# Performance work log

Measured on AMD Instinct MI355X. Metric: run time of the kernel, lower is better.

## Reference

```python
import jax, jax.numpy as jnp
import numpy as np

B, S, EMB, HID, IMG, ATT, K, HL = 64, 512, 768, 512, 2048, 512, 6, 20


def setup_inputs() -> dict:
    key = jax.random.key(0)
    ks = jax.random.split(key, 14)
    u = lambda k, shape: jax.random.uniform(k, shape, jnp.float32, -0.1, 0.1)
    return {
        "representations": jax.random.normal(ks[0], (B, S, EMB), jnp.float32),
        "lengths": jax.random.randint(ks[1], (B,), 0, S),
        "separate_images": jax.random.normal(ks[2], (B, K, IMG), jnp.float32),
        "visual_context": jax.random.normal(ks[3], (B, K * IMG), jnp.float32),
        "prev_hist": jax.random.normal(ks[4], (B, K, HL, EMB), jnp.float32),
        "hist_counts": jax.random.randint(ks[5], (B, K), 0, HL + 1),
        "masks": jax.random.randint(ks[6], (B, S, 1), 0, 2).astype(bool),
        "W_sep": u(ks[7], (IMG, HID)), "b_sep": jnp.zeros((HID,), jnp.float32),
        "W_e2h": u(ks[8], (EMB, HID)), "b_e2h": jnp.zeros((HID,), jnp.float32),
        "W_hist": u(ks[9], (EMB, HID)), "b_hist": jnp.zeros((HID,), jnp.float32),
        "W_ctx": u(ks[10], (K * IMG, HID)), "b_ctx": jnp.zeros((HID,), jnp.float32),
        "W_mm": u(ks[11], (2 * HID, HID)), "b_mm": jnp.zeros((HID,), jnp.float32),
        "W_a1": u(ks[12], (HID, ATT)), "b_a1": jnp.zeros((ATT,), jnp.float32),
        "W_a2": u(ks[13], (ATT, 1)), "b_a2": jnp.zeros((1,), jnp.float32),
    }


def reference(representations, lengths, separate_images, visual_context,
              prev_hist, hist_counts, masks,
              W_sep, b_sep, W_e2h, b_e2h, W_hist, b_hist, W_ctx, b_ctx,
              W_mm, b_mm, W_a1, b_a1, W_a2, b_a2):
    # dropout_prob = 0 -> dropout is identity (eval-mode equivalence)
    input_reps = jax.nn.relu(representations @ W_e2h + b_e2h)          # [B,S,H]
    ctx = jax.nn.relu(visual_context @ W_ctx + b_ctx)                  # [B,H]
    ctx_rep = jnp.broadcast_to(ctx[:, None, :], input_reps.shape)
    mm = jax.nn.relu(jnp.concatenate([input_reps, ctx_rep], -1) @ W_mm + b_mm)  # [B,S,H]
    scores = jnp.tanh(mm @ W_a1 + b_a1) @ W_a2 + b_a2                  # [B,S,1]
    scores = jnp.where(masks, -jnp.inf, scores)
    att_w = jax.nn.softmax(scores, axis=1)                             # softmax over seq
    attended = jnp.sum(mm * att_w, axis=1)                             # [B,H]

    sep = separate_images @ W_sep + b_sep                              # [B,K,H]
    hl = prev_hist.shape[2]
    valid = jnp.arange(hl)[None, None, :] < hist_counts[:, :, None]    # [B,K,HL]
    hsum = jnp.sum(prev_hist * valid[..., None].astype(prev_hist.dtype), axis=2)
    havg = hsum / jnp.maximum(hist_counts, 1)[..., None].astype(prev_hist.dtype)
    hproj = jax.nn.relu(havg @ W_hist + b_hist)                        # [B,K,H]
    sep = sep + jnp.where((hist_counts > 0)[..., None], hproj, 0.0)
    sep = jax.nn.relu(sep)
    # F.normalize(p=2, dim=2, eps=1e-12)
    sep = sep / jnp.maximum(jnp.linalg.norm(sep, axis=2, keepdims=True), 1e-12)
    dot = jnp.einsum('bkh,bh->bk', sep, attended)[..., None]           # [B,K,1]
    return dot
```

## Files before the change

kernel.cpp:

```cpp
#include <hip/hip_runtime.h>
#include <math.h>

#define B_    64
#define S_    512
#define EMB_  768
#define HID_  512
#define IMG_  2048
#define ATT_  512
#define K_    6
#define HL_   20
#define MS_   (B_ * S_)

typedef __attribute__((ext_vector_type(8))) short bf16x8;
typedef __attribute__((ext_vector_type(4))) float f32x4;

__device__ __forceinline__ unsigned short f2b(float f) {
    unsigned int u = __float_as_uint(f);
    u += 0x7fffu + ((u >> 16) & 1u);
    return (unsigned short)(u >> 16);
}
__device__ __forceinline__ unsigned int pk_bf16(float lo, float hi) {
    unsigned int r;
    asm volatile("v_cvt_pk_bf16_f32 %0, %1, %2" : "=v"(r) : "v"(lo), "v"(hi));
    return r;
}

#define GLD_LDS16(gp, lp)                                                        \
    __builtin_amdgcn_global_load_lds(                                            \
        (const __attribute__((address_space(1))) void*)(gp),                     \
        (__attribute__((address_space(3))) void*)(lp), 16, 0, 0)

__global__ __launch_bounds__(256)
void prep(const float* __restrict__ W_e2h, const float* __restrict__ W_mm,
          const float* __restrict__ W_a1,
          unsigned short* __restrict__ WtE2H, unsigned short* __restrict__ WtMM,
          unsigned short* __restrict__ WtA1,
          const unsigned char* __restrict__ masks, int* __restrict__ flag) {
    const int z = blockIdx.z;
    if (z == 3) {
        if (blockIdx.x != 0 || blockIdx.y != 0) return;
        __shared__ int found;
        if (threadIdx.x == 0) found = 0;
        __syncthreads();
        for (int i = threadIdx.x; i < 8192; i += 256)
            if ((i & 3) != 0 && masks[i] != 0) found = 1;
        __syncthreads();
        if (threadIdx.x == 0) *flag = found;
        return;
    }
    const float* W;
    unsigned short* Wt;
    int Kd;
    if (z == 0)      { W = W_e2h; Wt = WtE2H; Kd = EMB_; }
    else if (z == 1) { W = W_mm;  Wt = WtMM;  Kd = HID_; }
    else             { W = W_a1;  Wt = WtA1;  Kd = HID_; }
    if ((int)blockIdx.x * 32 >= Kd) return;

    __shared__ float tile[32][33];
    int k0 = blockIdx.x * 32, n0 = blockIdx.y * 32;
    int tx = threadIdx.x & 31, ty = threadIdx.x >> 5;
    #pragma unroll
    for (int i = 0; i < 4; ++i)
        tile[ty + i * 8][tx] = W[(size_t)(k0 + ty + i * 8) * HID_ + n0 + tx];
    __syncthreads();
    #pragma unroll
    for (int i = 0; i < 4; ++i)
        Wt[(size_t)(n0 + ty + i * 8) * Kd + k0 + tx] = f2b(tile[tx][ty + i * 8]);
}

__device__ __forceinline__ void tile_coords(int N, int& bm, int& bn) {
    const int nwg = gridDim.x;
    const int cpx = nwg >> 3;
    const int lid = ((int)blockIdx.x & 7) * cpx + ((int)blockIdx.x >> 3);
    const int ntl = N >> 7;
    bn = (lid % ntl) << 7;
    bm = (lid / ntl) << 7;
}

template<int ACT>
__global__ __launch_bounds__(256)
void gemm_bf16(const unsigned short* __restrict__ A, const unsigned short* __restrict__ Bt,
               const float* __restrict__ bias, const float* __restrict__ row_add,
               int row_div, unsigned short* __restrict__ Co, int M, int N, int Kd) {
    __shared__ unsigned short Als[2][128 * 64];
    __shared__ unsigned short Bls[2][128 * 64];
    const int tid = threadIdx.x;
    int bm, bn; tile_coords(N, bm, bn);
    const int lane = tid & 63, wid = tid >> 6;
    const int wr = wid >> 1, wc = wid & 1;
    const int fr = lane & 15, hi = lane >> 4;

    f32x4 acc[4][4] = {};
    int srow[4], scol[4];
    #pragma unroll
    for (int c = 0; c < 4; ++c) {
        int g = c * 256 + tid;
        srow[c] = g >> 3;
        scol[c] = (g & 7) ^ (srow[c] & 7);
    }

    const int nt = Kd >> 6;
    #pragma unroll
    for (int c = 0; c < 4; ++c) {
        int g = c * 256 + tid;
        GLD_LDS16(A + (size_t)(bm + srow[c]) * Kd + scol[c] * 8, &Als[0][g * 8]);
        GLD_LDS16(Bt + (size_t)(bn + srow[c]) * Kd + scol[c] * 8, &Bls[0][g * 8]);
    }
    __syncthreads();

    for (int t = 0; t < nt; ++t) {
        const int buf = t & 1;
        if (t + 1 < nt) {
            const int k0 = (t + 1) << 6;
            #pragma unroll
            for (int c = 0; c < 4; ++c) {
                int g = c * 256 + tid;
                GLD_LDS16(A + (size_t)(bm + srow[c]) * Kd + k0 + scol[c] * 8,
                          &Als[buf ^ 1][g * 8]);
                GLD_LDS16(Bt + (size_t)(bn + srow[c]) * Kd + k0 + scol[c] * 8,
                          &Bls[buf ^ 1][g * 8]);
            }
        }
        #pragma unroll
        for (int kk = 0; kk < 2; ++kk) {
            bf16x8 af[4], bv[4];
            #pragma unroll
            for (int m = 0; m < 4; ++m) {
                int row = wr * 64 + m * 16 + fr;
                int sc = (kk * 4 + hi) ^ (fr & 7);
                af[m] = *(const bf16x8*)&Als[buf][row * 64 + sc * 8];
            }
            #pragma unroll
            for (int n = 0; n < 4; ++n) {
                int row = wc * 64 + n * 16 + fr;
                int sc = (kk * 4 + hi) ^ (fr & 7);
                bv[n] = *(const bf16x8*)&Bls[buf][row * 64 + sc * 8];
            }
            #pragma unroll
            for (int m = 0; m < 4; ++m)
                #pragma unroll
                for (int n = 0; n < 4; ++n)
                    acc[m][n] = __builtin_amdgcn_mfma_f32_16x16x32_bf16(af[m], bv[n], acc[m][n], 0, 0, 0);
        }
        __syncthreads();
    }

    #pragma unroll
    for (int m = 0; m < 4; ++m) {
        #pragma unroll
        for (int n = 0; n < 4; ++n) {
            int col = bn + wc * 64 + n * 16 + fr;
            float badd = bias ? bias[col] : 0.f;
            #pragma unroll
            for (int r = 0; r < 4; ++r) {
                int row = bm + wr * 64 + m * 16 + hi * 4 + r;
                float x = acc[m][n][r] + badd;
                if (row_add) x += row_add[(size_t)(row / row_div) * N + col];
                if (ACT == 1) x = fmaxf(x, 0.f);
                if (ACT == 2) x = tanhf(x);
                Co[(size_t)row * N + col] = f2b(x);
            }
        }
    }
}

template<int ACT>
__global__ __launch_bounds__(256)
void gemm_f32in(const float* __restrict__ A, const unsigned short* __restrict__ Bt,
                const float* __restrict__ bias, unsigned short* __restrict__ Co,
                int M, int N, int Kd) {
    __shared__ unsigned short Als[2][128 * 64];
    __shared__ unsigned short Bls[2][128 * 64];
    const int tid = threadIdx.x;
    int bm, bn; tile_coords(N, bm, bn);
    const int lane = tid & 63, wid = tid >> 6;
    const int wr = wid >> 1, wc = wid & 1;
    const int fr = lane & 15, hi = lane >> 4;

    f32x4 acc[4][4] = {};
    int srow[4], lcol[4], scol[4];
    #pragma unroll
    for (int c = 0; c < 4; ++c) {
        int g = c * 256 + tid;
        srow[c] = g >> 3;
        lcol[c] = g & 7;
        scol[c] = lcol[c] ^ (srow[c] & 7);
    }

    const int nt = Kd >> 6;
    float4 ra[8];

    #pragma unroll
    for (int c = 0; c < 4; ++c) {
        int g = c * 256 + tid;
        GLD_LDS16(Bt + (size_t)(bn + srow[c]) * Kd + scol[c] * 8, &Bls[0][g * 8]);
        const float* p = A + (size_t)(bm + srow[c]) * Kd + lcol[c] * 8;
        ra[2 * c]     = *(const float4*)p;
        ra[2 * c + 1] = *(const float4*)(p + 4);
    }
    #pragma unroll
    for (int c = 0; c < 4; ++c) {
        uint4 u;
        u.x = pk_bf16(ra[2*c].x,   ra[2*c].y);
        u.y = pk_bf16(ra[2*c].z,   ra[2*c].w);
        u.z = pk_bf16(ra[2*c+1].x, ra[2*c+1].y);
        u.w = pk_bf16(ra[2*c+1].z, ra[2*c+1].w);
        *(uint4*)&Als[0][(srow[c] * 8 + scol[c]) * 8] = u;
    }
    __syncthreads();

    for (int t = 0; t < nt; ++t) {
        const int buf = t & 1;
        if (t + 1 < nt) {
            const int k0 = (t + 1) << 6;
            #pragma unroll
            for (int c = 0; c < 4; ++c) {
                int g = c * 256 + tid;
                GLD_LDS16(Bt + (size_t)(bn + srow[c]) * Kd + k0 + scol[c] * 8,
                          &Bls[buf ^ 1][g * 8]);
                const float* p = A + (size_t)(bm + srow[c]) * Kd + k0 + lcol[c] * 8;
                ra[2 * c]     = *(const float4*)p;
                ra[2 * c + 1] = *(const float4*)(p + 4);
            }
        }
        #pragma unroll
        for (int kk = 0; kk < 2; ++kk) {
            bf16x8 af[4], bv[4];
            #pragma unroll
            for (int m = 0; m < 4; ++m) {
                int row = wr * 64 + m * 16 + fr;
                int sc = (kk * 4 + hi) ^ (fr & 7);
                af[m] = *(const bf16x8*)&Als[buf][row * 64 + sc * 8];
            }
            #pragma unroll
            for (int n = 0; n < 4; ++n) {
                int row = wc * 64 + n * 16 + fr;
                int sc = (kk * 4 + hi) ^ (fr & 7);
                bv[n] = *(const bf16x8*)&Bls[buf][row * 64 + sc * 8];
            }
            #pragma unroll
            for (int m = 0; m < 4; ++m)
                #pragma unroll
                for (int n = 0; n < 4; ++n)
                    acc[m][n] = __builtin_amdgcn_mfma_f32_16x16x32_bf16(af[m], bv[n], acc[m][n], 0, 0, 0);
        }
        if (t + 1 < nt) {
            #pragma unroll
            for (int c = 0; c < 4; ++c) {
                uint4 u;
                u.x = pk_bf16(ra[2*c].x,   ra[2*c].y);
                u.y = pk_bf16(ra[2*c].z,   ra[2*c].w);
                u.z = pk_bf16(ra[2*c+1].x, ra[2*c+1].y);
                u.w = pk_bf16(ra[2*c+1].z, ra[2*c+1].w);
                *(uint4*)&Als[buf ^ 1][(srow[c] * 8 + scol[c]) * 8] = u;
            }
        }
        __syncthreads();
    }

    #pragma unroll
    for (int m = 0; m < 4; ++m) {
        #pragma unroll
        for (int n = 0; n < 4; ++n) {
            int col = bn + wc * 64 + n * 16 + fr;
            float badd = bias ? bias[col] : 0.f;
            #pragma unroll
            for (int r = 0; r < 4; ++r) {
                int row = bm + wr * 64 + m * 16 + hi * 4 + r;
                float x = acc[m][n][r] + badd;
                if (ACT == 1) x = fmaxf(x, 0.f);
                Co[(size_t)row * N + col] = f2b(x);
            }
        }
    }
}

__global__ __launch_bounds__(256)
void gemm_score(const unsigned short* __restrict__ A, const unsigned short* __restrict__ Bt,
                const float* __restrict__ b_a1, const float* __restrict__ W_a2,
                float* __restrict__ scores8, int M, int N, int Kd) {
    __shared__ unsigned short Als[2][128 * 64];
    __shared__ unsigned short Bls[2][128 * 64];
    const int tid = threadIdx.x;
    int bm, bn; tile_coords(N, bm, bn);
    const int lane = tid & 63, wid = tid >> 6;
    const int wr = wid >> 1, wc = wid & 1;
    const int fr = lane & 15, hi = lane >> 4;

    f32x4 acc[4][4] = {};
    int srow[4], scol[4];
    #pragma unroll
    for (int c = 0; c < 4; ++c) {
        int g = c * 256 + tid;
        srow[c] = g >> 3;
        scol[c] = (g & 7) ^ (srow[c] & 7);
    }

    const int nt = Kd >> 6;
    #pragma unroll
    for (int c = 0; c < 4; ++c) {
        int g = c * 256 + tid;
        GLD_LDS16(A + (size_t)(bm + srow[c]) * Kd + scol[c] * 8, &Als[0][g * 8]);
        GLD_LDS16(Bt + (size_t)(bn + srow[c]) * Kd + scol[c] * 8, &Bls[0][g * 8]);
    }
    __syncthreads();

    for (int t = 0; t < nt; ++t) {
        const int buf = t & 1;
        if (t + 1 < nt) {
            const int k0 = (t + 1) << 6;
            #pragma unroll
            for (int c = 0; c < 4; ++c) {
                int g = c * 256 + tid;
                GLD_LDS16(A + (size_t)(bm + srow[c]) * Kd + k0 + scol[c] * 8,
                          &Als[buf ^ 1][g * 8]);
                GLD_LDS16(Bt + (size_t)(bn + srow[c]) * Kd + k0 + scol[c] * 8,
                          &Bls[buf ^ 1][g * 8]);
            }
        }
        #pragma unroll
        for (int kk = 0; kk < 2; ++kk) {
            bf16x8 af[4], bv[4];
            #pragma unroll
            for (int m = 0; m < 4; ++m) {
                int row = wr * 64 + m * 16 + fr;
                int sc = (kk * 4 + hi) ^ (fr & 7);
                af[m] = *(const bf16x8*)&Als[buf][row * 64 + sc * 8];
            }
            #pragma unroll
            for (int n = 0; n < 4; ++n) {
                int row = wc * 64 + n * 16 + fr;
                int sc = (kk * 4 + hi) ^ (fr & 7);
                bv[n] = *(const bf16x8*)&Bls[buf][row * 64 + sc * 8];
            }
            #pragma unroll
            for (int m = 0; m < 4; ++m)
                #pragma unroll
                for (int n = 0; n < 4; ++n)
                    acc[m][n] = __builtin_amdgcn_mfma_f32_16x16x32_bf16(af[m], bv[n], acc[m][n], 0, 0, 0);
        }
        __syncthreads();
    }

    float ba[4], wa[4];
    #pragma unroll
    for (int n = 0; n < 4; ++n) {
        int col = bn + wc * 64 + n * 16 + fr;
        ba[n] = b_a1[col];
        wa[n] = W_a2[col];
    }
    const int slot = (bn >> 7) * 2 + wc;
    #pragma unroll
    for (int m = 0; m < 4; ++m) {
        #pragma unroll
        for (int r = 0; r < 4; ++r) {
            float p = 0.f;
            #pragma unroll
            for (int n = 0; n < 4; ++n)
                p += tanhf(acc[m][n][r] + ba[n]) * wa[n];
            p += __shfl_xor(p, 1, 64);
            p += __shfl_xor(p, 2, 64);
            p += __shfl_xor(p, 4, 64);
            p += __shfl_xor(p, 8, 64);
            if (fr == 0)
                scores8[(size_t)slot * M + bm + wr * 64 + m * 16 + hi * 4 + r] = p;
        }
    }
}

__global__ __launch_bounds__(256)
void gemm_splitk(const float* __restrict__ A, const float* __restrict__ W,
                 float* __restrict__ P, int M, int N, int Kd, int kps) {
    __shared__ float As[16][68];
    __shared__ float Ws[16][64];
    const int tid = threadIdx.x;
    const int bm = blockIdx.y * 64, bn = blockIdx.x * 64;
    const int ks = blockIdx.z;
    const int tx = tid & 15, ty = tid >> 4;
    const int arow = tid >> 2, akq = tid & 3;
    const int wk = tid >> 4, wnq = tid & 15;

    float acc[4][4] = {};
    const int kbeg = ks * kps, kend = kbeg + kps;

    for (int k0 = kbeg; k0 < kend; k0 += 16) {
        float4 av = *(const float4*)&A[(size_t)(bm + arow) * Kd + k0 + akq * 4];
        float4 wv = *(const float4*)&W[(size_t)(k0 + wk) * N + bn + wnq * 4];
        As[akq * 4 + 0][arow] = av.x;
        As[akq * 4 + 1][arow] = av.y;
        As[akq * 4 + 2][arow] = av.z;
        As[akq * 4 + 3][arow] = av.w;
        *(float4*)&Ws[wk][wnq * 4] = wv;
        __syncthreads();
        #pragma unroll
        for (int kk = 0; kk < 16; ++kk) {
            float4 a4 = *(const float4*)&As[kk][ty * 4];
            float4 b4 = *(const float4*)&Ws[kk][tx * 4];
            float a_[4] = {a4.x, a4.y, a4.z, a4.w};
            float b_[4] = {b4.x, b4.y, b4.z, b4.w};
            #pragma unroll
            for (int i = 0; i < 4; ++i)
                #pragma unroll
                for (int j = 0; j < 4; ++j)
                    acc[i][j] += a_[i] * b_[j];
        }
        __syncthreads();
    }

    float* Pbase = P + (size_t)ks * M * N;
    #pragma unroll
    for (int i = 0; i < 4; ++i) {
        int row = bm + ty * 4 + i;
        float4 v = {acc[i][0], acc[i][1], acc[i][2], acc[i][3]};
        *(float4*)&Pbase[(size_t)row * N + bn + tx * 4] = v;
    }
}

template<int ACT>
__global__ __launch_bounds__(256)
void reduce_k(const float* __restrict__ P, const float* __restrict__ bias,
              float* __restrict__ C, int MN, int N, int nsplit) {
    int idx = blockIdx.x * 256 + threadIdx.x;
    if (idx >= MN) return;
    float s = 0.f;
    for (int z = 0; z < nsplit; ++z) s += P[(size_t)z * MN + idx];
    if (bias) s += bias[idx & (N - 1)];
    if (ACT == 1) s = fmaxf(s, 0.f);
    C[idx] = s;
}

__global__ __launch_bounds__(256)
void softmax8(const float* __restrict__ scores8, const float* __restrict__ b_a2,
              const void* __restrict__ masks_raw, const int* __restrict__ flag,
              float* __restrict__ attw) {
    int b = blockIdx.x, tid = threadIdx.x;
    bool isb = (*flag) != 0;
    const unsigned char* mb = (const unsigned char*)masks_raw;
    const int* mi = (const int*)masks_raw;
    int lane = tid & 63, wv = tid >> 6;
    __shared__ float red[4], red2[4];
    float bias = b_a2[0];

    float m = -INFINITY;
    for (int s = tid; s < S_; s += 256) {
        int idx = b * S_ + s;
        float v = bias;
        #pragma unroll
        for (int z = 0; z < 8; ++z) v += scores8[(size_t)z * MS_ + idx];
        bool mk = isb ? (mb[idx] != 0) : (mi[idx] != 0);
        v = mk ? -INFINITY : v;
        attw[idx] = v;
        m = fmaxf(m, v);
    }
    #pragma unroll
    for (int off = 32; off; off >>= 1) m = fmaxf(m, __shfl_down(m, off, 64));
    if (lane == 0) red[wv] = m;
    __syncthreads();
    if (tid == 0) red[0] = fmaxf(fmaxf(red[0], red[1]), fmaxf(red[2], red[3]));
    __syncthreads();
    float Mx = red[0];

    float sum = 0.f;
    for (int s = tid; s < S_; s += 256) {
        int idx = b * S_ + s;
        float e = expf(attw[idx] - Mx);
        attw[idx] = e;
        sum += e;
    }
    #pragma unroll
    for (int off = 32; off; off >>= 1) sum += __shfl_down(sum, off, 64);
    if (lane == 0) red2[wv] = sum;
    __syncthreads();
    if (tid == 0) red2[0] = red2[0] + red2[1] + red2[2] + red2[3];
    __syncthreads();
    float inv = 1.f / red2[0];
    for (int s = tid; s < S_; s += 256) attw[b * S_ + s] *= inv;
}

__global__ __launch_bounds__(256)
void attended4(const unsigned short* __restrict__ mm, const float* __restrict__ attw,
               float* __restrict__ att4) {
    int b = blockIdx.x;
    int h = blockIdx.y * 256 + threadIdx.x;
    int z = blockIdx.z;
    __shared__ float w[128];
    int s0 = z * 128;
    if (threadIdx.x < 128) w[threadIdx.x] = attw[b * S_ + s0 + threadIdx.x];
    __syncthreads();
    float acc = 0.f;
    for (int s = 0; s < 128; ++s)
        acc += __uint_as_float((unsigned int)mm[((size_t)b * S_ + s0 + s) * HID_ + h] << 16) * w[s];
    att4[((size_t)z * B_ + b) * HID_ + h] = acc;
}

__global__ __launch_bounds__(256)
void hist_avg(const float* __restrict__ ph, const int* __restrict__ hcnt,
              float* __restrict__ havg) {
    int bk = blockIdx.x;
    int cnt = hcnt[bk];
    float denom = (float)(cnt > 1 ? cnt : 1);
    const float* base = ph + (size_t)bk * HL_ * EMB_;
    for (int e = threadIdx.x; e < EMB_; e += 256) {
        float s = 0.f;
        for (int l = 0; l < cnt; ++l) s += base[l * EMB_ + e];
        havg[bk * EMB_ + e] = s / denom;
    }
}

__global__ __launch_bounds__(256)
void combine_all(const float* __restrict__ skA, const float* __restrict__ skB,
                 const float* __restrict__ b_hist, const float* __restrict__ b_sep,
                 const int* __restrict__ hcnt, const float* __restrict__ att4,
                 float* __restrict__ out) {
    const int MNA = B_ * K_ * HID_;
    int bk = blockIdx.x, tid = threadIdx.x;
    int b = bk / K_;
    int cnt = hcnt[bk];
    float sq = 0.f, dt = 0.f;
    #pragma unroll
    for (int i = 0; i < HID_ / 256; ++i) {
        int h = tid + i * 256;
        size_t idx = (size_t)bk * HID_ + h;
        float hp = b_hist[h];
        #pragma unroll
        for (int z = 0; z < 8; ++z) hp += skA[(size_t)z * MNA + idx];
        hp = fmaxf(hp, 0.f);
        float sp = b_sep[h];
        #pragma unroll
        for (int z = 0; z < 16; ++z) sp += skB[(size_t)z * MNA + idx];
        float v = sp + (cnt > 0 ? hp : 0.f);
        v = fmaxf(v, 0.f);
        float at = 0.f;
        #pragma unroll
        for (int z = 0; z < 4; ++z) at += att4[((size_t)z * B_ + b) * HID_ + h];
        sq += v * v;
        dt += v * at;
    }
    #pragma unroll
    for (int off = 32; off; off >>= 1) {
        sq += __shfl_down(sq, off, 64);
        dt += __shfl_down(dt, off, 64);
    }
    __shared__ float rs[4], rd[4];
    int lane = tid & 63, wv = tid >> 6;
    if (lane == 0) { rs[wv] = sq; rd[wv] = dt; }
    __syncthreads();
    if (tid == 0) {
        float Sq = rs[0] + rs[1] + rs[2] + rs[3];
        float Dt = rd[0] + rd[1] + rd[2] + rd[3];
        float norm = fmaxf(sqrtf(Sq), 1e-12f);
        out[bk] = Dt / norm;
    }
}

extern "C" void kernel_launch(void* const* d_in, const int* in_sizes, int n_in,
                              void* d_out, int out_size, void* d_ws, size_t ws_size,
                              hipStream_t stream) {
    const float* reps     = (const float*)d_in[0];
    const float* sep_imgs = (const float*)d_in[2];
    const float* vctx     = (const float*)d_in[3];
    const float* phist    = (const float*)d_in[4];
    const int*   hcnt     = (const int*)d_in[5];
    const void*  masks    = d_in[6];
    const float* W_sep = (const float*)d_in[7];
    const float* b_sep = (const float*)d_in[8];
    const float* W_e2h = (const float*)d_in[9];
    const float* b_e2h = (const float*)d_in[10];
    const float* W_hist = (const float*)d_in[11];
    const float* b_hist = (const float*)d_in[12];
    const float* W_ctx = (const float*)d_in[13];
    const float* b_ctx = (const float*)d_in[14];
    const float* W_mm = (const float*)d_in[15];
    const float* b_mm = (const float*)d_in[16];
    const float* W_a1 = (const float*)d_in[17];
    const float* b_a1 = (const float*)d_in[18];
    const float* W_a2 = (const float*)d_in[19];
    const float* b_a2 = (const float*)d_in[20];
    float* out = (float*)d_out;

    const size_t MS = (size_t)MS_;
    const int MNA = B_ * K_ * HID_;

    unsigned short* actA  = (unsigned short*)d_ws;
    unsigned short* actB  = actA + MS * HID_;
    unsigned short* WtE2H = actB + MS * HID_;
    unsigned short* WtMM  = WtE2H + (size_t)EMB_ * HID_;
    unsigned short* WtA1  = WtMM + (size_t)HID_ * HID_;
    float* skC    = (float*)(WtA1 + (size_t)HID_ * HID_);
    float* skA    = skC + (size_t)64 * B_ * HID_;
    float* skB    = skA + (size_t)8 * MNA;
    float* scores8 = skB + (size_t)16 * MNA;
    float* attw   = scores8 + 8 * MS;
    float* att4   = attw + MS;
    float* ctx    = att4 + (size_t)4 * B_ * HID_;
    float* ctx2   = ctx + B_ * HID_;
    float* havg   = ctx2 + B_ * HID_;
    int*   flag   = (int*)(havg + (size_t)B_ * K_ * EMB_);

    prep<<<dim3(EMB_ / 32, HID_ / 32, 4), 256, 0, stream>>>(
        W_e2h, W_mm, W_a1, WtE2H, WtMM, WtA1, (const unsigned char*)masks, flag);

    {
        const int nsp = 64, kps = (K_ * IMG_) / nsp;
        gemm_splitk<<<dim3(8, 1, nsp), 256, 0, stream>>>(vctx, W_ctx, skC,
                                                         B_, HID_, K_ * IMG_, kps);
        reduce_k<1><<<(B_ * HID_ + 255) / 256, 256, 0, stream>>>(skC, b_ctx, ctx,
                                                                 B_ * HID_, HID_, nsp);
    }
    {
        const int nsp = 8, kps = HID_ / nsp;
        gemm_splitk<<<dim3(8, 1, nsp), 256, 0, stream>>>(ctx, W_mm + (size_t)HID_ * HID_,
                                                         skC, B_, HID_, HID_, kps);
        reduce_k<0><<<(B_ * HID_ + 255) / 256, 256, 0, stream>>>(skC, b_mm, ctx2,
                                                                 B_ * HID_, HID_, nsp);
    }

    const int big_grid = (MS_ / 128) * (HID_ / 128);
    gemm_f32in<1><<<big_grid, 256, 0, stream>>>(reps, WtE2H, b_e2h, actA,
                                                MS_, HID_, EMB_);
    gemm_bf16<1><<<big_grid, 256, 0, stream>>>(actA, WtMM, nullptr, ctx2, S_,
                                               actB, MS_, HID_, HID_);
    gemm_score<<<big_grid, 256, 0, stream>>>(actB, WtA1, b_a1, W_a2, scores8,
                                             MS_, ATT_, HID_);
    softmax8<<<B_, 256, 0, stream>>>(scores8, b_a2, masks, flag, attw);
    attended4<<<dim3(B_, HID_ / 256, 4), 256, 0, stream>>>(actB, attw, att4);
    hist_avg<<<B_ * K_, 256, 0, stream>>>(phist, hcnt, havg);
    gemm_splitk<<<dim3(8, 6, 8), 256, 0, stream>>>(havg, W_hist, skA,
                                                   B_ * K_, HID_, EMB_, EMB_ / 8);
    gemm_splitk<<<dim3(8, 6, 16), 256, 0, stream>>>(sep_imgs, W_sep, skB,
                                                    B_ * K_, HID_, IMG_, IMG_ / 16);
    combine_all<<<B_ * K_, 256, 0, stream>>>(skA, skB, b_hist, b_sep, hcnt,
                                             att4, out);
}
```

Measured before the change: 262.7 us.

## Replace LDS-staged GEMMs with direct global-to-register MFMA operand loads

The three big GEMMs drop shared-memory staging and barriers. Each lane now loads its MFMA A and B fragments straight from global memory into registers, with two register sets double-buffered and s_setprio raised around the MFMA bursts. The three kernels are unified into one template, and launch bounds now target 2 blocks per CU. This removes LDS traffic and __syncthreads stalls, but each wave loses cross-wave operand reuse, so it leans on L1/L2 for the shared tiles and reads with a less coalesced 16-byte-per-lane pattern.

```diff
diff --git a/kernel.cpp b/kernel.cpp
--- a/kernel.cpp
+++ b/kernel.cpp
@@ -24,11 +24,14 @@
     asm volatile("v_cvt_pk_bf16_f32 %0, %1, %2" : "=v"(r) : "v"(lo), "v"(hi));
     return r;
 }
-
-#define GLD_LDS16(gp, lp)                                                        \
-    __builtin_amdgcn_global_load_lds(                                            \
-        (const __attribute__((address_space(1))) void*)(gp),                     \
-        (__attribute__((address_space(3))) void*)(lp), 16, 0, 0)
+__device__ __forceinline__ bf16x8 cvt8(const float4& x, const float4& y) {
+    union { unsigned int u[4]; bf16x8 v; } r;
+    r.u[0] = pk_bf16(x.x, x.y);
+    r.u[1] = pk_bf16(x.z, x.w);
+    r.u[2] = pk_bf16(y.x, y.y);
+    r.u[3] = pk_bf16(y.z, y.w);
+    return r.v;
+}
 
 __global__ __launch_bounds__(256)
 void prep(const float* __restrict__ W_e2h, const float* __restrict__ W_mm,
@@ -77,293 +80,115 @@
     bm = (lid / ntl) << 7;
 }
 
-template<int ACT>
-__global__ __launch_bounds__(256)
-void gemm_bf16(const unsigned short* __restrict__ A, const unsigned short* __restrict__ Bt,
-               const float* __restrict__ bias, const float* __restrict__ row_add,
-               int row_div, unsigned short* __restrict__ Co, int M, int N, int Kd) {
-    __shared__ unsigned short Als[2][128 * 64];
-    __shared__ unsigned short Bls[2][128 * 64];
+template<bool AF32, int ACT, bool SCORE>
+__global__ __launch_bounds__(256, 2)
+void gemm_nolds(const void* __restrict__ Av, const unsigned short* __restrict__ Bt,
+                const float* __restrict__ bias, const float* __restrict__ row_add,
+                int row_div, unsigned short* __restrict__ Co,
+                const float* __restrict__ W_a2, float* __restrict__ scores8,
+                int M, int N, int Kd) {
     const int tid = threadIdx.x;
     int bm, bn; tile_coords(N, bm, bn);
     const int lane = tid & 63, wid = tid >> 6;
     const int wr = wid >> 1, wc = wid & 1;
     const int fr = lane & 15, hi = lane >> 4;
 
+    const float* pAf[4];
+    const unsigned short* pA[4];
+    const unsigned short* pB[4];
+    #pragma unroll
+    for (int m = 0; m < 4; ++m) {
+        size_t off = (size_t)(bm + wr * 64 + m * 16 + fr) * Kd + hi * 8;
+        pAf[m] = (const float*)Av + off;
+        pA[m]  = (const unsigned short*)Av + off;
+    }
+    #pragma unroll
+    for (int n = 0; n < 4; ++n)
+        pB[n] = Bt + (size_t)(bn + wc * 64 + n * 16 + fr) * Kd + hi * 8;
+
     f32x4 acc[4][4] = {};
-    int srow[4], scol[4];
-    #pragma unroll
-    for (int c = 0; c < 4; ++c) {
-        int g = c * 256 + tid;
-        srow[c] = g >> 3;
-        scol[c] = (g & 7) ^ (srow[c] & 7);
-    }
-
-    const int nt = Kd >> 6;
-    #pragma unroll
-    for (int c = 0; c < 4; ++c) {
-        int g = c * 256 + tid;
-        GLD_LDS16(A + (size_t)(bm + srow[c]) * Kd + scol[c] * 8, &Als[0][g * 8]);
-        GLD_LDS16(Bt + (size_t)(bn + srow[c]) * Kd + scol[c] * 8, &Bls[0][g * 8]);
-    }
-    __syncthreads();
-
-    for (int t = 0; t < nt; ++t) {
-        const int buf = t & 1;
-        if (t + 1 < nt) {
-            const int k0 = (t + 1) << 6;
-            #pragma unroll
-            for (int c = 0; c < 4; ++c) {
-                int g = c * 256 + tid;
-                GLD_LDS16(A + (size_t)(bm + srow[c]) * Kd + k0 + scol[c] * 8,
-                          &Als[buf ^ 1][g * 8]);
-                GLD_LDS16(Bt + (size_t)(bn + srow[c]) * Kd + k0 + scol[c] * 8,
-                          &Bls[buf ^ 1][g * 8]);
+    bf16x8 a0[4], a1[4], b0[4], b1[4];
+    float4 f0[4][2], f1[4][2];
+
+    auto load_set = [&](bf16x8 (&AS)[4], float4 (&FS)[4][2], bf16x8 (&BS)[4], int kc) {
+        #pragma unroll
+        for (int m = 0; m < 4; ++m) {
+            if (AF32) {
+                FS[m][0] = *(const float4*)(pAf[m] + kc);
+                FS[m][1] = *(const float4*)(pAf[m] + kc + 4);
+            } else {
+                AS[m] = *(const bf16x8*)(pA[m] + kc);
             }
         }
         #pragma unroll
-        for (int kk = 0; kk < 2; ++kk) {
-            bf16x8 af[4], bv[4];
+        for (int n = 0; n < 4; ++n) BS[n] = *(const bf16x8*)(pB[n] + kc);
+    };
+    auto compute_set = [&](bf16x8 (&AS)[4], float4 (&FS)[4][2], bf16x8 (&BS)[4]) {
+        bf16x8 av[4];
+        #pragma unroll
+        for (int m = 0; m < 4; ++m)
+            av[m] = AF32 ? cvt8(FS[m][0], FS[m][1]) : AS[m];
+        __builtin_amdgcn_s_setprio(1);
+        #pragma unroll
+        for (int m = 0; m < 4; ++m)
             #pragma unroll
-            for (int m = 0; m < 4; ++m) {
-                int row = wr * 64 + m * 16 + fr;
-                int sc = (kk * 4 + hi) ^ (fr & 7);
-                af[m] = *(const bf16x8*)&Als[buf][row * 64 + sc * 8];
+            for (int n = 0; n < 4; ++n)
+                acc[m][n] = __builtin_amdgcn_mfma_f32_16x16x32_bf16(av[m], BS[n], acc[m][n], 0, 0, 0);
+        __builtin_amdgcn_s_setprio(0);
+    };
+
+    const int half = Kd >> 6;
+    load_set(a0, f0, b0, 0);
+    load_set(a1, f1, b1, 32);
+    for (int i = 0; i < half; ++i) {
+        const int kc = i << 6;
+        compute_set(a0, f0, b0);
+        if (i + 1 < half) load_set(a0, f0, b0, kc + 64);
+        compute_set(a1, f1, b1);
+        if (i + 1 < half) load_set(a1, f1, b1, kc + 96);
+    }
+
+    if (SCORE) {
+        float ba[4], wa[4];
+        #pragma unroll
+        for (int n = 0; n < 4; ++n) {
+            int col = bn + wc * 64 + n * 16 + fr;
+            ba[n] = bias[col];
+            wa[n] = W_a2[col];
+        }
+        const int slot = (bn >> 7) * 2 + wc;
+        #pragma unroll
+        for (int m = 0; m < 4; ++m) {
+            #pragma unroll
+            for (int r = 0; r < 4; ++r) {
+                float p = 0.f;
+                #pragma unroll
+                for (int n = 0; n < 4; ++n)
+                    p += tanhf(acc[m][n][r] + ba[n]) * wa[n];
+                p += __shfl_xor(p, 1, 64);
+                p += __shfl_xor(p, 2, 64);
+                p += __shfl_xor(p, 4, 64);
+                p += __shfl_xor(p, 8, 64);
+                if (fr == 0)
+                    scores8[(size_t)slot * M + bm + wr * 64 + m * 16 + hi * 4 + r] = p;
             }
+        }
+    } else {
+        #pragma unroll
+        for (int m = 0; m < 4; ++m) {
             #pragma unroll
             for (int n = 0; n < 4; ++n) {
-                int row = wc * 64 + n * 16 + fr;
-                int sc = (kk * 4 + hi) ^ (fr & 7);
-                bv[n] = *(const bf16x8*)&Bls[buf][row * 64 + sc * 8];
+                int col = bn + wc * 64 + n * 16 + fr;
+                float badd = bias ? bias[col] : 0.f;
+                #pragma unroll
+                for (int r = 0; r < 4; ++r) {
+                    int row = bm + wr * 64 + m * 16 + hi * 4 + r;
+                    float x = acc[m][n][r] + badd;
+                    if (row_add) x += row_add[(size_t)(row / row_div) * N + col];
+                    if (ACT == 1) x = fmaxf(x, 0.f);
+                    Co[(size_t)row * N + col] = f2b(x);
+                }
             }
-            #pragma unroll
-            for (int m = 0; m < 4; ++m)
-                #pragma unroll
-                for (int n = 0; n < 4; ++n)
-                    acc[m][n] = __builtin_amdgcn_mfma_f32_16x16x32_bf16(af[m], bv[n], acc[m][n], 0, 0, 0);
-        }
-        __syncthreads();
-    }
-
-    #pragma unroll
-    for (int m = 0; m < 4; ++m) {
-        #pragma unroll
-        for (int n = 0; n < 4; ++n) {
-            int col = bn + wc * 64 + n * 16 + fr;
-            float badd = bias ? bias[col] : 0.f;
-            #pragma unroll
-            for (int r = 0; r < 4; ++r) {
-                int row = bm + wr * 64 + m * 16 + hi * 4 + r;
-                float x = acc[m][n][r] + badd;
-                if (row_add) x += row_add[(size_t)(row / row_div) * N + col];
-                if (ACT == 1) x = fmaxf(x, 0.f);
-                if (ACT == 2) x = tanhf(x);
-                Co[(size_t)row * N + col] = f2b(x);
-            }
-        }
-    }
-}
-
-template<int ACT>
-__global__ __launch_bounds__(256)
-void gemm_f32in(const float* __restrict__ A, const unsigned short* __restrict__ Bt,
-                const float* __restrict__ bias, unsigned short* __restrict__ Co,
-                int M, int N, int Kd) {
-    __shared__ unsigned short Als[2][128 * 64];
-    __shared__ unsigned short Bls[2][128 * 64];
-    const int tid = threadIdx.x;
-    int bm, bn; tile_coords(N, bm, bn);
-    const int lane = tid & 63, wid = tid >> 6;
-    const int wr = wid >> 1, wc = wid & 1;
-    const int fr = lane & 15, hi = lane >> 4;
-
-    f32x4 acc[4][4] = {};
-    int srow[4], lcol[4], scol[4];
-    #pragma unroll
-    for (int c = 0; c < 4; ++c) {
-        int g = c * 256 + tid;
-        srow[c] = g >> 3;
-        lcol[c] = g & 7;
-        scol[c] = lcol[c] ^ (srow[c] & 7);
-    }
-
-    const int nt = Kd >> 6;
-    float4 ra[8];
-
-    #pragma unroll
-    for (int c = 0; c < 4; ++c) {
-        int g = c * 256 + tid;
-        GLD_LDS16(Bt + (size_t)(bn + srow[c]) * Kd + scol[c] * 8, &Bls[0][g * 8]);
-        const float* p = A + (size_t)(bm + srow[c]) * Kd + lcol[c] * 8;
-        ra[2 * c]     = *(const float4*)p;
-        ra[2 * c + 1] = *(const float4*)(p + 4);
-    }
-    #pragma unroll
-    for (int c = 0; c < 4; ++c) {
-        uint4 u;
-        u.x = pk_bf16(ra[2*c].x,   ra[2*c].y);
-        u.y = pk_bf16(ra[2*c].z,   ra[2*c].w);
-        u.z = pk_bf16(ra[2*c+1].x, ra[2*c+1].y);
-        u.w = pk_bf16(ra[2*c+1].z, ra[2*c+1].w);
-        *(uint4*)&Als[0][(srow[c] * 8 + scol[c]) * 8] = u;
-    }
-    __syncthreads();
-
-    for (int t = 0; t < nt; ++t) {
-        const int buf = t & 1;
-        if (t + 1 < nt) {
-            const int k0 = (t + 1) << 6;
-            #pragma unroll
-            for (int c = 0; c < 4; ++c) {
-                int g = c * 256 + tid;
-                GLD_LDS16(Bt + (size_t)(bn + srow[c]) * Kd + k0 + scol[c] * 8,
-                          &Bls[buf ^ 1][g * 8]);
-                const float* p = A + (size_t)(bm + srow[c]) * Kd + k0 + lcol[c] * 8;
-                ra[2 * c]     = *(const float4*)p;
-                ra[2 * c + 1] = *(const float4*)(p + 4);
-            }
-        }
-        #pragma unroll
-        for (int kk = 0; kk < 2; ++kk) {
-            bf16x8 af[4], bv[4];
-            #pragma unroll
-            for (int m = 0; m < 4; ++m) {
-                int row = wr * 64 + m * 16 + fr;
-                int sc = (kk * 4 + hi) ^ (fr & 7);
-                af[m] = *(const bf16x8*)&Als[buf][row * 64 + sc * 8];
-            }
-            #pragma unroll
-            for (int n = 0; n < 4; ++n) {
-                int row = wc * 64 + n * 16 + fr;
-                int sc = (kk * 4 + hi) ^ (fr & 7);
-                bv[n] = *(const bf16x8*)&Bls[buf][row * 64 + sc * 8];
-            }
-            #pragma unroll
-            for (int m = 0; m < 4; ++m)
-                #pragma unroll
-                for (int n = 0; n < 4; ++n)
-                    acc[m][n] = __builtin_amdgcn_mfma_f32_16x16x32_bf16(af[m], bv[n], acc[m][n], 0, 0, 0);
-        }
-        if (t + 1 < nt) {
-            #pragma unroll
-            for (int c = 0; c < 4; ++c) {
-                uint4 u;
-                u.x = pk_bf16(ra[2*c].x,   ra[2*c].y);
-                u.y = pk_bf16(ra[2*c].z,   ra[2*c].w);
-                u.z = pk_bf16(ra[2*c+1].x, ra[2*c+1].y);
-                u.w = pk_bf16(ra[2*c+1].z, ra[2*c+1].w);
-                *(uint4*)&Als[buf ^ 1][(srow[c] * 8 + scol[c]) * 8] = u;
-            }
-        }
-        __syncthreads();
-    }
-
-    #pragma unroll
-    for (int m = 0; m < 4; ++m) {
-        #pragma unroll
-        for (int n = 0; n < 4; ++n) {
-            int col = bn + wc * 64 + n * 16 + fr;
-            float badd = bias ? bias[col] : 0.f;
-            #pragma unroll
-            for (int r = 0; r < 4; ++r) {
-                int row = bm + wr * 64 + m * 16 + hi * 4 + r;
-                float x = acc[m][n][r] + badd;
-                if (ACT == 1) x = fmaxf(x, 0.f);
-                Co[(size_t)row * N + col] = f2b(x);
-            }
-        }
-    }
-}
-
-__global__ __launch_bounds__(256)
-void gemm_score(const unsigned short* __restrict__ A, const unsigned short* __restrict__ Bt,
-                const float* __restrict__ b_a1, const float* __restrict__ W_a2,
-                float* __restrict__ scores8, int M, int N, int Kd) {
-    __shared__ unsigned short Als[2][128 * 64];
-    __shared__ unsigned short Bls[2][128 * 64];
-    const int tid = threadIdx.x;
-    int bm, bn; tile_coords(N, bm, bn);
-    const int lane = tid & 63, wid = tid >> 6;
-    const int wr = wid >> 1, wc = wid & 1;
-    const int fr = lane & 15, hi = lane >> 4;
-
-    f32x4 acc[4][4] = {};
-    int srow[4], scol[4];
-    #pragma unroll
-    for (int c = 0; c < 4; ++c) {
-        int g = c * 256 + tid;
-        srow[c] = g >> 3;
-        scol[c] = (g & 7) ^ (srow[c] & 7);
-    }
-
-    const int nt = Kd >> 6;
-    #pragma unroll
-    for (int c = 0; c < 4; ++c) {
-        int g = c * 256 + tid;
-        GLD_LDS16(A + (size_t)(bm + srow[c]) * Kd + scol[c] * 8, &Als[0][g * 8]);
-        GLD_LDS16(Bt + (size_t)(bn + srow[c]) * Kd + scol[c] * 8, &Bls[0][g * 8]);
-    }
-    __syncthreads();
-
-    for (int t = 0; t < nt; ++t) {
-        const int buf = t & 1;
-        if (t + 1 < nt) {
-            const int k0 = (t + 1) << 6;
-            #pragma unroll
-            for (int c = 0; c < 4; ++c) {
-                int g = c * 256 + tid;
-                GLD_LDS16(A + (size_t)(bm + srow[c]) * Kd + k0 + scol[c] * 8,
-                          &Als[buf ^ 1][g * 8]);
-                GLD_LDS16(Bt + (size_t)(bn + srow[c]) * Kd + k0 + scol[c] * 8,
-                          &Bls[buf ^ 1][g * 8]);
-            }
-        }
-        #pragma unroll
-        for (int kk = 0; kk < 2; ++kk) {
-            bf16x8 af[4], bv[4];
-            #pragma unroll
-            for (int m = 0; m < 4; ++m) {
-                int row = wr * 64 + m * 16 + fr;
-                int sc = (kk * 4 + hi) ^ (fr & 7);
-                af[m] = *(const bf16x8*)&Als[buf][row * 64 + sc * 8];
-            }
-            #pragma unroll
-            for (int n = 0; n < 4; ++n) {
-                int row = wc * 64 + n * 16 + fr;
-                int sc = (kk * 4 + hi) ^ (fr & 7);
-                bv[n] = *(const bf16x8*)&Bls[buf][row * 64 + sc * 8];
-            }
-            #pragma unroll
-            for (int m = 0; m < 4; ++m)
-                #pragma unroll
-                for (int n = 0; n < 4; ++n)
-                    acc[m][n] = __builtin_amdgcn_mfma_f32_16x16x32_bf16(af[m], bv[n], acc[m][n], 0, 0, 0);
-        }
-        __syncthreads();
-    }
-
-    float ba[4], wa[4];
-    #pragma unroll
-    for (int n = 0; n < 4; ++n) {
-        int col = bn + wc * 64 + n * 16 + fr;
-        ba[n] = b_a1[col];
-        wa[n] = W_a2[col];
-    }
-    const int slot = (bn >> 7) * 2 + wc;
-    #pragma unroll
-    for (int m = 0; m < 4; ++m) {
-        #pragma unroll
-        for (int r = 0; r < 4; ++r) {
-            float p = 0.f;
-            #pragma unroll
-            for (int n = 0; n < 4; ++n)
-                p += tanhf(acc[m][n][r] + ba[n]) * wa[n];
-            p += __shfl_xor(p, 1, 64);
-            p += __shfl_xor(p, 2, 64);
-            p += __shfl_xor(p, 4, 64);
-            p += __shfl_xor(p, 8, 64);
-            if (fr == 0)
-                scores8[(size_t)slot * M + bm + wr * 64 + m * 16 + hi * 4 + r] = p;
         }
     }
 }
@@ -616,12 +441,12 @@
     }
 
     const int big_grid = (MS_ / 128) * (HID_ / 128);
-    gemm_f32in<1><<<big_grid, 256, 0, stream>>>(reps, WtE2H, b_e2h, actA,
-                                                MS_, HID_, EMB_);
-    gemm_bf16<1><<<big_grid, 256, 0, stream>>>(actA, WtMM, nullptr, ctx2, S_,
-                                               actB, MS_, HID_, HID_);
-    gemm_score<<<big_grid, 256, 0, stream>>>(actB, WtA1, b_a1, W_a2, scores8,
-                                             MS_, ATT_, HID_);
+    gemm_nolds<true, 1, false><<<big_grid, 256, 0, stream>>>(
+        reps, WtE2H, b_e2h, nullptr, 1, actA, nullptr, nullptr, MS_, HID_, EMB_);
+    gemm_nolds<false, 1, false><<<big_grid, 256, 0, stream>>>(
+        actA, WtMM, nullptr, ctx2, S_, actB, nullptr, nullptr, MS_, HID_, HID_);
+    gemm_nolds<false, 0, true><<<big_grid, 256, 0, stream>>>(
+        actB, WtA1, b_a1, nullptr, 1, actA, W_a2, scores8, MS_, ATT_, HID_);
     softmax8<<<B_, 256, 0, stream>>>(scores8, b_a2, masks, flag, attw);
     attended4<<<dim3(B_, HID_ / 256, 4), 256, 0, stream>>>(actB, attw, att4);
     hist_avg<<<B_ * K_, 256, 0, stream>>>(phist, hcnt, havg);
```

Result: slower. 414.2 us (+57.7%).
